# Kernel optimization log

Hardware: AMD Instinct MI355X
Metric: run time of the kernel (lower is better)

## Reference

```python
import jax, jax.numpy as jnp
import numpy as np

# Dimensions
B, S = 4, 1024            # sequences, tokens per sequence (prefill: q_len == kv_len)
NQO, NKV, D = 32, 8, 128  # GQA heads
BS = 16                   # page (block) size
NUM_BLOCKS = 512
BLOCKS_PER_SEQ = S // BS  # 64
SCALE = 1.0 / float(np.sqrt(D))


def setup_inputs() -> dict:
    key = jax.random.key(0)
    k1, k2, k3 = jax.random.split(key, 3)
    query = jax.random.normal(k1, (B * S, NQO * D), dtype=jnp.float32)
    key_t = jax.random.normal(k2, (B * S, NKV * D), dtype=jnp.float32)
    value = jax.random.normal(k3, (B * S, NKV * D), dtype=jnp.float32)

    # Paged layout: each sequence owns BLOCKS_PER_SEQ distinct blocks (shuffled).
    rng = np.random.default_rng(0)
    perm = rng.permutation(NUM_BLOCKS)[: B * BLOCKS_PER_SEQ]
    block_tables = perm.reshape(B, BLOCKS_PER_SEQ).astype(np.int32)
    tok = np.arange(S)
    # flat slot index for token t of sequence b: block_id * BS + offset
    slots = block_tables[:, tok // BS] * BS + (tok % BS)  # [B, S]
    new_cache_slots = jnp.asarray(slots.reshape(-1), dtype=jnp.int32)

    key_cache = jnp.zeros((NUM_BLOCKS, BS, NKV, D), dtype=jnp.float32)
    value_cache = jnp.zeros((NUM_BLOCKS, BS, NKV, D), dtype=jnp.float32)
    return {
        "query": query,
        "key": key_t,
        "value": value,
        "key_cache": key_cache,
        "value_cache": value_cache,
        "new_cache_slots": new_cache_slots,
        "block_tables": jnp.asarray(block_tables),
    }


def reference(query, key, value, key_cache, value_cache, new_cache_slots, block_tables):
    q = query.reshape(B * S, NQO, D)
    k = key.reshape(B * S, NKV, D)
    v = value.reshape(B * S, NKV, D)

    # Scatter new K/V into paged cache (kv_cache.set_kv_cache)
    kc = key_cache.reshape(NUM_BLOCKS * BS, NKV, D).at[new_cache_slots].set(k)
    vc = value_cache.reshape(NUM_BLOCKS * BS, NKV, D).at[new_cache_slots].set(v)

    # Gather per-sequence contiguous KV via block tables
    slot = (block_tables[:, :, None] * BS + jnp.arange(BS)).reshape(B, S)  # [B,S]
    kseq = kc[slot]  # [B, S, NKV, D]
    vseq = vc[slot]  # [B, S, NKV, D]

    G = NQO // NKV
    qb = q.reshape(B, S, NKV, G, D)
    scores = jnp.einsum("bqhgd,bkhd->bhgqk", qb, kseq) * SCALE

    # causal mask (q_len == kv_len here; general rule: k_pos <= kv_len - q_len + q_pos)
    qpos = jnp.arange(S)[:, None]
    kpos = jnp.arange(S)[None, :]
    scores = jnp.where(qpos >= kpos, scores, -jnp.inf)

    probs = jax.nn.softmax(scores, axis=-1)
    out = jnp.einsum("bhgqk,bkhd->bqhgd", probs, vseq)
    return out.reshape(B * S, NQO * D)
```

## Files before the change

kernel.cpp:

```cpp
#include <hip/hip_runtime.h>

typedef __attribute__((ext_vector_type(8))) short bf16x8;
typedef __attribute__((ext_vector_type(16))) float f32x16;
typedef __attribute__((ext_vector_type(4))) unsigned uint4v;
typedef __attribute__((ext_vector_type(2))) unsigned uint2v;

#define MFMA32(a, b, c) __builtin_amdgcn_mfma_f32_32x32x16_bf16((a), (b), (c), 0, 0, 0)

__device__ __forceinline__ unsigned pk2(float lo, float hi) {
  unsigned r;
  asm("v_cvt_pk_bf16_f32 %0, %1, %2" : "=v"(r) : "v"(lo), "v"(hi));
  return r;
}

__device__ __forceinline__ float fexp2(float x) {
  float y; asm("v_exp_f32 %0, %1" : "=v"(y) : "v"(x)); return y;
}

__device__ __forceinline__ f32x16 zero16() {
  f32x16 z;
#pragma unroll
  for (int i = 0; i < 16; ++i) z[i] = 0.0f;
  return z;
}

constexpr int S_ = 1024, D = 128;
constexpr int QSTR = 32 * 128;
constexpr int KSTR = 8 * 128;
constexpr float QSCL = 0.12751741f;

__global__ __launch_bounds__(512, 2) void fa_kernel(
    const float* __restrict__ Qg, const float* __restrict__ Kg,
    const float* __restrict__ Vg, float* __restrict__ Og) {
  const int bid  = blockIdx.x;
  const int hkv  = bid & 7;
  const int b    = (bid >> 3) & 3;
  const int qt64 = 15 - (bid >> 5);
  const int h4   = hkv << 2;

  const int tid  = threadIdx.x;
  const int wid  = tid >> 6;
  const int lane = tid & 63;
  const int r    = lane & 31;
  const int hi   = lane >> 5;

  const int g     = wid & 3;
  const int strip = wid >> 2;
  const int h     = h4 + g;
  const int wq0   = (qt64 << 6) + (strip << 5);
  const int qrow  = wq0 + r;

  __shared__ __align__(16) unsigned char Kl0[64 * 256];
  __shared__ __align__(16) unsigned char Vl0[128 * 128];
  __shared__ __align__(16) unsigned char Kl1[64 * 256];
  __shared__ __align__(16) unsigned char Vl1[128 * 128];

  bf16x8 qf[8];
  {
    const float* qp = Qg + (size_t)(b * S_ + qrow) * QSTR + h * D;
#pragma unroll
    for (int c = 0; c < 8; ++c) {
      const float4* p4 = (const float4*)(qp + 16 * c + 8 * hi);
      float4 x = p4[0], y = p4[1];
      uint4v w = (uint4v){pk2(x.x * QSCL, x.y * QSCL), pk2(x.z * QSCL, x.w * QSCL),
                          pk2(y.x * QSCL, y.y * QSCL), pk2(y.z * QSCL, y.w * QSCL)};
      qf[c] = __builtin_bit_cast(bf16x8, w);
    }
  }

  const int kvrow = tid >> 3;
  const int dbase = (tid & 7) << 4;
  const float* kbase = Kg + (size_t)(b * S_) * KSTR + hkv * D;
  const int vd   = tid & 127;
  const int vkvb = (tid >> 7) << 4;
  const float* vbase = Vg + (size_t)(b * S_) * KSTR + hkv * D;

  float4 kreg[4];
  float  vreg[16];

  auto ISSUE = [&](int kv0) {
    const float4* kp = (const float4*)(kbase + (size_t)(kv0 + kvrow) * KSTR + dbase);
#pragma unroll
    for (int j = 0; j < 4; ++j) kreg[j] = kp[j];
    const float* vp = vbase + (size_t)(kv0 + vkvb) * KSTR + vd;
#pragma unroll
    for (int kk = 0; kk < 16; ++kk) vreg[kk] = vp[kk * KSTR];
  };

  auto WRITE = [&](unsigned char* Kl, unsigned char* Vl) {
#pragma unroll
    for (int ss = 0; ss < 2; ++ss) {
      float4 x = kreg[2 * ss], y = kreg[2 * ss + 1];
      uint4v w = (uint4v){pk2(x.x, x.y), pk2(x.z, x.w), pk2(y.x, y.y), pk2(y.z, y.w)};
      const int slot = (dbase >> 3) + ss;
      *(uint4v*)(Kl + kvrow * 256 + ((slot ^ (kvrow & 7)) << 4)) = w;
    }
#pragma unroll
    for (int ss = 0; ss < 2; ++ss) {
      uint4v w = (uint4v){pk2(vreg[8 * ss + 0], vreg[8 * ss + 1]),
                          pk2(vreg[8 * ss + 2], vreg[8 * ss + 3]),
                          pk2(vreg[8 * ss + 4], vreg[8 * ss + 5]),
                          pk2(vreg[8 * ss + 6], vreg[8 * ss + 7])};
      const int slot = (vkvb >> 3) + ss;
      *(uint4v*)(Vl + vd * 128 + ((slot ^ (vd & 7)) << 4)) = w;
    }
  };

  f32x16 o0 = zero16(), o1 = zero16(), o2 = zero16(), o3 = zero16();
  float m = -1e30f, lsum = 0.0f;

  auto COMPUTE = [&](const unsigned char* Kl, const unsigned char* Vl, int kv0) {
    f32x16 s0 = zero16(), s1 = zero16();
    __builtin_amdgcn_s_setprio(1);
#pragma unroll
    for (int c = 0; c < 8; ++c) {
      const int so = (((2 * c + hi) ^ (r & 7)) << 4);
      bf16x8 k0 = *(const bf16x8*)(Kl + r * 256 + so);
      bf16x8 k1 = *(const bf16x8*)(Kl + (32 + r) * 256 + so);
      s0 = MFMA32(k0, qf[c], s0);
      s1 = MFMA32(k1, qf[c], s1);
    }
    __builtin_amdgcn_s_setprio(0);

    if (kv0 + 63 > wq0) {
#pragma unroll
      for (int rr = 0; rr < 16; ++rr) {
        const int R = (rr & 3) + ((rr >> 2) << 3) + (hi << 2);
        if (kv0 + R > qrow)      s0[rr] = -1e30f;
        if (kv0 + 32 + R > qrow) s1[rr] = -1e30f;
      }
    }

    float mx[8];
#pragma unroll
    for (int rr = 0; rr < 8; ++rr)
      mx[rr] = fmaxf(fmaxf(s0[rr], s0[rr + 8]), fmaxf(s1[rr], s1[rr + 8]));
#pragma unroll
    for (int rr = 0; rr < 4; ++rr) mx[rr] = fmaxf(mx[rr], mx[rr + 4]);
    float mt = fmaxf(fmaxf(mx[0], mx[1]), fmaxf(mx[2], mx[3]));
    mt = fmaxf(mt, __shfl_xor(mt, 32));

    if (__any(mt > m + 6.0f)) {
      const float mn = fmaxf(m, mt);
      const float sc = fexp2(m - mn);
      m = mn;
      lsum *= sc;
#pragma unroll
      for (int rr = 0; rr < 16; ++rr) {
        const float srow = __shfl(sc, (rr & 3) + ((rr >> 2) << 3) + (hi << 2));
        o0[rr] *= srow; o1[rr] *= srow; o2[rr] *= srow; o3[rr] *= srow;
      }
    }

    float ps0 = 0.0f, ps1 = 0.0f, ps2 = 0.0f, ps3 = 0.0f;
    bf16x8 A0, A1, A2, A3;
    {
      float p[16];
#pragma unroll
      for (int rr = 0; rr < 16; ++rr) { p[rr] = fexp2(s0[rr] - m); }
#pragma unroll
      for (int rr = 0; rr < 4; ++rr) {
        ps0 += p[4 * rr + 0]; ps1 += p[4 * rr + 1];
        ps2 += p[4 * rr + 2]; ps3 += p[4 * rr + 3];
      }
      unsigned d0 = pk2(p[0], p[1]),   d1 = pk2(p[2], p[3]);
      unsigned d2 = pk2(p[4], p[5]),   d3 = pk2(p[6], p[7]);
      unsigned d4 = pk2(p[8], p[9]),   d5 = pk2(p[10], p[11]);
      unsigned d6 = pk2(p[12], p[13]), d7 = pk2(p[14], p[15]);
      uint2v w02 = __builtin_amdgcn_permlane32_swap(d0, d2, false, false);
      uint2v w13 = __builtin_amdgcn_permlane32_swap(d1, d3, false, false);
      uint2v w46 = __builtin_amdgcn_permlane32_swap(d4, d6, false, false);
      uint2v w57 = __builtin_amdgcn_permlane32_swap(d5, d7, false, false);
      A0 = __builtin_bit_cast(bf16x8, (uint4v){w02[0], w13[0], w02[1], w13[1]});
      A1 = __builtin_bit_cast(bf16x8, (uint4v){w46[0], w57[0], w46[1], w57[1]});
    }
    {
      float p[16];
#pragma unroll
      for (int rr = 0; rr < 16; ++rr) { p[rr] = fexp2(s1[rr] - m); }
#pragma unroll
      for (int rr = 0; rr < 4; ++rr) {
        ps0 += p[4 * rr + 0]; ps1 += p[4 * rr + 1];
        ps2 += p[4 * rr + 2]; ps3 += p[4 * rr + 3];
      }
      unsigned d0 = pk2(p[0], p[1]),   d1 = pk2(p[2], p[3]);
      unsigned d2 = pk2(p[4], p[5]),   d3 = pk2(p[6], p[7]);
      unsigned d4 = pk2(p[8], p[9]),   d5 = pk2(p[10], p[11]);
      unsigned d6 = pk2(p[12], p[13]), d7 = pk2(p[14], p[15]);
      uint2v w02 = __builtin_amdgcn_permlane32_swap(d0, d2, false, false);
      uint2v w13 = __builtin_amdgcn_permlane32_swap(d1, d3, false, false);
      uint2v w46 = __builtin_amdgcn_permlane32_swap(d4, d6, false, false);
      uint2v w57 = __builtin_amdgcn_permlane32_swap(d5, d7, false, false);
      A2 = __builtin_bit_cast(bf16x8, (uint4v){w02[0], w13[0], w02[1], w13[1]});
      A3 = __builtin_bit_cast(bf16x8, (uint4v){w46[0], w57[0], w46[1], w57[1]});
    }
    lsum += (ps0 + ps1) + (ps2 + ps3);

    __builtin_amdgcn_s_setprio(1);
#pragma unroll
    for (int t = 0; t < 4; ++t) {
      const bf16x8 pf = (t == 0) ? A0 : (t == 1) ? A1 : (t == 2) ? A2 : A3;
      const int so = (((2 * t + hi) ^ (r & 7)) << 4);
      bf16x8 v0 = *(const bf16x8*)(Vl + r * 128 + so);
      bf16x8 v1 = *(const bf16x8*)(Vl + (32 + r) * 128 + so);
      bf16x8 v2 = *(const bf16x8*)(Vl + (64 + r) * 128 + so);
      bf16x8 v3 = *(const bf16x8*)(Vl + (96 + r) * 128 + so);
      o0 = MFMA32(pf, v0, o0);
      o1 = MFMA32(pf, v1, o1);
      o2 = MFMA32(pf, v2, o2);
      o3 = MFMA32(pf, v3, o3);
    }
    __builtin_amdgcn_s_setprio(0);
  };

  const int nt = qt64 + 1;

  ISSUE(0);
  WRITE(Kl0, Vl0);
  if (nt > 1) ISSUE(64);

  unsigned char *Kc = Kl0, *Vc = Vl0, *Kn = Kl1, *Vn = Vl1;
  for (int t = 0; t < nt; ++t) {
    __syncthreads();
    if (wid < 4) {
      COMPUTE(Kc, Vc, t << 6);
      if (t + 1 < nt) {
        WRITE(Kn, Vn);
        if (t + 2 < nt) ISSUE((t + 2) << 6);
      }
    } else {
      if (t + 1 < nt) {
        WRITE(Kn, Vn);
        if (t + 2 < nt) ISSUE((t + 2) << 6);
      }
      COMPUTE(Kc, Vc, t << 6);
    }
    if (t + 1 < nt) {
      unsigned char* tp;
      tp = Kc; Kc = Kn; Kn = tp;
      tp = Vc; Vc = Vn; Vn = tp;
    }
  }

  float lt = lsum + __shfl_xor(lsum, 32);
#pragma unroll
  for (int rr = 0; rr < 16; ++rr) {
    const int R = (rr & 3) + ((rr >> 2) << 3) + (hi << 2);
    const float li = __shfl(lt, R);
    const float inv = 1.0f / li;
    float* op = Og + (size_t)(b * S_ + wq0 + R) * QSTR + h * D + r;
    op[0]  = o0[rr] * inv;
    op[32] = o1[rr] * inv;
    op[64] = o2[rr] * inv;
    op[96] = o3[rr] * inv;
  }
}

extern "C" void kernel_launch(void* const* d_in, const int* in_sizes, int n_in,
                              void* d_out, int out_size, void* d_ws, size_t ws_size,
                              hipStream_t stream) {
  const float* Q = (const float*)d_in[0];
  const float* K = (const float*)d_in[1];
  const float* V = (const float*)d_in[2];
  float* O = (float*)d_out;
  fa_kernel<<<dim3(512), dim3(512), 0, stream>>>(Q, K, V, O);
}
```

Before: 61.24 us.

## Split KV tile softmax into two 32-key halves to overlap exp with MFMA

Restructures the per-tile compute so the first 32-key score block goes through its own masking, online-softmax max/rescale, exp and PV MFMAs before the second half is processed. The intent is to let the exp/pack work of one half interleave with the matrix work of the other and to shorten register live ranges. In exchange there are two max reductions and possible rescale passes per 64-key tile instead of one, which adds VALU work and shuffles.

```diff
diff --git a/kernel.cpp b/kernel.cpp
--- a/kernel.cpp
+++ b/kernel.cpp
@@ -116,53 +116,54 @@
     for (int c = 0; c < 8; ++c) {
       const int so = (((2 * c + hi) ^ (r & 7)) << 4);
       bf16x8 k0 = *(const bf16x8*)(Kl + r * 256 + so);
+      s0 = MFMA32(k0, qf[c], s0);
+    }
+#pragma unroll
+    for (int c = 0; c < 8; ++c) {
+      const int so = (((2 * c + hi) ^ (r & 7)) << 4);
       bf16x8 k1 = *(const bf16x8*)(Kl + (32 + r) * 256 + so);
-      s0 = MFMA32(k0, qf[c], s0);
       s1 = MFMA32(k1, qf[c], s1);
     }
     __builtin_amdgcn_s_setprio(0);
 
-    if (kv0 + 63 > wq0) {
+    if (kv0 + 31 > wq0) {
 #pragma unroll
       for (int rr = 0; rr < 16; ++rr) {
         const int R = (rr & 3) + ((rr >> 2) << 3) + (hi << 2);
-        if (kv0 + R > qrow)      s0[rr] = -1e30f;
-        if (kv0 + 32 + R > qrow) s1[rr] = -1e30f;
-      }
-    }
-
-    float mx[8];
-#pragma unroll
-    for (int rr = 0; rr < 8; ++rr)
-      mx[rr] = fmaxf(fmaxf(s0[rr], s0[rr + 8]), fmaxf(s1[rr], s1[rr + 8]));
-#pragma unroll
-    for (int rr = 0; rr < 4; ++rr) mx[rr] = fmaxf(mx[rr], mx[rr + 4]);
-    float mt = fmaxf(fmaxf(mx[0], mx[1]), fmaxf(mx[2], mx[3]));
-    mt = fmaxf(mt, __shfl_xor(mt, 32));
-
-    if (__any(mt > m + 6.0f)) {
-      const float mn = fmaxf(m, mt);
-      const float sc = fexp2(m - mn);
-      m = mn;
-      lsum *= sc;
-#pragma unroll
-      for (int rr = 0; rr < 16; ++rr) {
-        const float srow = __shfl(sc, (rr & 3) + ((rr >> 2) << 3) + (hi << 2));
-        o0[rr] *= srow; o1[rr] *= srow; o2[rr] *= srow; o3[rr] *= srow;
-      }
-    }
-
-    float ps0 = 0.0f, ps1 = 0.0f, ps2 = 0.0f, ps3 = 0.0f;
-    bf16x8 A0, A1, A2, A3;
+        if (kv0 + R > qrow) s0[rr] = -1e30f;
+      }
+    }
+    {
+      float mx[8];
+#pragma unroll
+      for (int rr = 0; rr < 8; ++rr) mx[rr] = fmaxf(s0[rr], s0[rr + 8]);
+#pragma unroll
+      for (int rr = 0; rr < 4; ++rr) mx[rr] = fmaxf(mx[rr], mx[rr + 4]);
+      float mt = fmaxf(fmaxf(mx[0], mx[1]), fmaxf(mx[2], mx[3]));
+      mt = fmaxf(mt, __shfl_xor(mt, 32));
+      if (__any(mt > m + 6.0f)) {
+        const float mn = fmaxf(m, mt);
+        const float sc = fexp2(m - mn);
+        m = mn;
+        lsum *= sc;
+#pragma unroll
+        for (int rr = 0; rr < 16; ++rr) {
+          const float srow = __shfl(sc, (rr & 3) + ((rr >> 2) << 3) + (hi << 2));
+          o0[rr] *= srow; o1[rr] *= srow; o2[rr] *= srow; o3[rr] *= srow;
+        }
+      }
+    }
     {
       float p[16];
 #pragma unroll
-      for (int rr = 0; rr < 16; ++rr) { p[rr] = fexp2(s0[rr] - m); }
+      for (int rr = 0; rr < 16; ++rr) p[rr] = fexp2(s0[rr] - m);
+      float ps0 = 0.0f, ps1 = 0.0f, ps2 = 0.0f, ps3 = 0.0f;
 #pragma unroll
       for (int rr = 0; rr < 4; ++rr) {
         ps0 += p[4 * rr + 0]; ps1 += p[4 * rr + 1];
         ps2 += p[4 * rr + 2]; ps3 += p[4 * rr + 3];
       }
+      lsum += (ps0 + ps1) + (ps2 + ps3);
       unsigned d0 = pk2(p[0], p[1]),   d1 = pk2(p[2], p[3]);
       unsigned d2 = pk2(p[4], p[5]),   d3 = pk2(p[6], p[7]);
       unsigned d4 = pk2(p[8], p[9]),   d5 = pk2(p[10], p[11]);
@@ -171,18 +172,63 @@
       uint2v w13 = __builtin_amdgcn_permlane32_swap(d1, d3, false, false);
       uint2v w46 = __builtin_amdgcn_permlane32_swap(d4, d6, false, false);
       uint2v w57 = __builtin_amdgcn_permlane32_swap(d5, d7, false, false);
-      A0 = __builtin_bit_cast(bf16x8, (uint4v){w02[0], w13[0], w02[1], w13[1]});
-      A1 = __builtin_bit_cast(bf16x8, (uint4v){w46[0], w57[0], w46[1], w57[1]});
+      bf16x8 A0 = __builtin_bit_cast(bf16x8, (uint4v){w02[0], w13[0], w02[1], w13[1]});
+      bf16x8 A1 = __builtin_bit_cast(bf16x8, (uint4v){w46[0], w57[0], w46[1], w57[1]});
+      __builtin_amdgcn_s_setprio(1);
+#pragma unroll
+      for (int t = 0; t < 2; ++t) {
+        const bf16x8 pf = (t == 0) ? A0 : A1;
+        const int so = (((2 * t + hi) ^ (r & 7)) << 4);
+        bf16x8 v0 = *(const bf16x8*)(Vl + r * 128 + so);
+        bf16x8 v1 = *(const bf16x8*)(Vl + (32 + r) * 128 + so);
+        bf16x8 v2 = *(const bf16x8*)(Vl + (64 + r) * 128 + so);
+        bf16x8 v3 = *(const bf16x8*)(Vl + (96 + r) * 128 + so);
+        o0 = MFMA32(pf, v0, o0);
+        o1 = MFMA32(pf, v1, o1);
+        o2 = MFMA32(pf, v2, o2);
+        o3 = MFMA32(pf, v3, o3);
+      }
+      __builtin_amdgcn_s_setprio(0);
+    }
+
+    if (kv0 + 63 > wq0) {
+#pragma unroll
+      for (int rr = 0; rr < 16; ++rr) {
+        const int R = (rr & 3) + ((rr >> 2) << 3) + (hi << 2);
+        if (kv0 + 32 + R > qrow) s1[rr] = -1e30f;
+      }
+    }
+    {
+      float mx[8];
+#pragma unroll
+      for (int rr = 0; rr < 8; ++rr) mx[rr] = fmaxf(s1[rr], s1[rr + 8]);
+#pragma unroll
+      for (int rr = 0; rr < 4; ++rr) mx[rr] = fmaxf(mx[rr], mx[rr + 4]);
+      float mt = fmaxf(fmaxf(mx[0], mx[1]), fmaxf(mx[2], mx[3]));
+      mt = fmaxf(mt, __shfl_xor(mt, 32));
+      if (__any(mt > m + 6.0f)) {
+        const float mn = fmaxf(m, mt);
+        const float sc = fexp2(m - mn);
+        m = mn;
+        lsum *= sc;
+#pragma unroll
+        for (int rr = 0; rr < 16; ++rr) {
+          const float srow = __shfl(sc, (rr & 3) + ((rr >> 2) << 3) + (hi << 2));
+          o0[rr] *= srow; o1[rr] *= srow; o2[rr] *= srow; o3[rr] *= srow;
+        }
+      }
     }
     {
       float p[16];
 #pragma unroll
-      for (int rr = 0; rr < 16; ++rr) { p[rr] = fexp2(s1[rr] - m); }
+      for (int rr = 0; rr < 16; ++rr) p[rr] = fexp2(s1[rr] - m);
+      float ps0 = 0.0f, ps1 = 0.0f, ps2 = 0.0f, ps3 = 0.0f;
 #pragma unroll
       for (int rr = 0; rr < 4; ++rr) {
         ps0 += p[4 * rr + 0]; ps1 += p[4 * rr + 1];
         ps2 += p[4 * rr + 2]; ps3 += p[4 * rr + 3];
       }
+      lsum += (ps0 + ps1) + (ps2 + ps3);
       unsigned d0 = pk2(p[0], p[1]),   d1 = pk2(p[2], p[3]);
       unsigned d2 = pk2(p[4], p[5]),   d3 = pk2(p[6], p[7]);
       unsigned d4 = pk2(p[8], p[9]),   d5 = pk2(p[10], p[11]);
@@ -191,26 +237,24 @@
       uint2v w13 = __builtin_amdgcn_permlane32_swap(d1, d3, false, false);
       uint2v w46 = __builtin_amdgcn_permlane32_swap(d4, d6, false, false);
       uint2v w57 = __builtin_amdgcn_permlane32_swap(d5, d7, false, false);
-      A2 = __builtin_bit_cast(bf16x8, (uint4v){w02[0], w13[0], w02[1], w13[1]});
-      A3 = __builtin_bit_cast(bf16x8, (uint4v){w46[0], w57[0], w46[1], w57[1]});
-    }
-    lsum += (ps0 + ps1) + (ps2 + ps3);
-
-    __builtin_amdgcn_s_setprio(1);
-#pragma unroll
-    for (int t = 0; t < 4; ++t) {
-      const bf16x8 pf = (t == 0) ? A0 : (t == 1) ? A1 : (t == 2) ? A2 : A3;
-      const int so = (((2 * t + hi) ^ (r & 7)) << 4);
-      bf16x8 v0 = *(const bf16x8*)(Vl + r * 128 + so);
-      bf16x8 v1 = *(const bf16x8*)(Vl + (32 + r) * 128 + so);
-      bf16x8 v2 = *(const bf16x8*)(Vl + (64 + r) * 128 + so);
-      bf16x8 v3 = *(const bf16x8*)(Vl + (96 + r) * 128 + so);
-      o0 = MFMA32(pf, v0, o0);
-      o1 = MFMA32(pf, v1, o1);
-      o2 = MFMA32(pf, v2, o2);
-      o3 = MFMA32(pf, v3, o3);
-    }
-    __builtin_amdgcn_s_setprio(0);
+      bf16x8 A2 = __builtin_bit_cast(bf16x8, (uint4v){w02[0], w13[0], w02[1], w13[1]});
+      bf16x8 A3 = __builtin_bit_cast(bf16x8, (uint4v){w46[0], w57[0], w46[1], w57[1]});
+      __builtin_amdgcn_s_setprio(1);
+#pragma unroll
+      for (int t = 2; t < 4; ++t) {
+        const bf16x8 pf = (t == 2) ? A2 : A3;
+        const int so = (((2 * t + hi) ^ (r & 7)) << 4);
+        bf16x8 v0 = *(const bf16x8*)(Vl + r * 128 + so);
+        bf16x8 v1 = *(const bf16x8*)(Vl + (32 + r) * 128 + so);
+        bf16x8 v2 = *(const bf16x8*)(Vl + (64 + r) * 128 + so);
+        bf16x8 v3 = *(const bf16x8*)(Vl + (96 + r) * 128 + so);
+        o0 = MFMA32(pf, v0, o0);
+        o1 = MFMA32(pf, v1, o1);
+        o2 = MFMA32(pf, v2, o2);
+        o3 = MFMA32(pf, v3, o3);
+      }
+      __builtin_amdgcn_s_setprio(0);
+    }
   };
 
   const int nt = qt64 + 1;
```

Result: slower. 63.97 us (+4.5%).
